# Kernel optimization log

Hardware: AMD Instinct MI355X
Metric: run time of the kernel (lower is better)

Reference implementation:

```python
import jax, jax.numpy as jnp
import numpy as np

N_NODES = 100000
N_EDGES = 1600000
IN_DIM = 128
HID = 64
N_CLASSES = 40
NEG_SLOPE = 0.2


def setup_inputs() -> dict:
    key = jax.random.key(0)
    ks = jax.random.split(key, 12)
    s_in = 1.0 / np.sqrt(IN_DIM)
    s_h = 1.0 / np.sqrt(HID)
    return {
        "x": jax.random.normal(ks[0], (N_NODES, IN_DIM), dtype=jnp.float32),
        "edge_index": jax.random.randint(ks[1], (2, N_EDGES), 0, N_NODES, dtype=jnp.int64),
        "W0": jax.random.normal(ks[2], (IN_DIM, HID), dtype=jnp.float32) * s_in,
        "a_s0": jax.random.normal(ks[3], (HID,), dtype=jnp.float32) * s_h,
        "a_d0": jax.random.normal(ks[4], (HID,), dtype=jnp.float32) * s_h,
        "b0": jnp.zeros((HID,), dtype=jnp.float32),
        "W1": jax.random.normal(ks[5], (HID, HID), dtype=jnp.float32) * s_h,
        "a_s1": jax.random.normal(ks[6], (HID,), dtype=jnp.float32) * s_h,
        "a_d1": jax.random.normal(ks[7], (HID,), dtype=jnp.float32) * s_h,
        "b1": jnp.zeros((HID,), dtype=jnp.float32),
        "Wl": jax.random.normal(ks[8], (HID, N_CLASSES), dtype=jnp.float32) * s_h,
        "bl": jnp.zeros((N_CLASSES,), dtype=jnp.float32),
    }


def gat_conv(x, src, dst, W, a_s, a_d, b, n_nodes):
    # single-head GATConv (PyG default heads=1), self-loops already in src/dst
    h = x @ W                                  # [N, d]
    e = jax.nn.leaky_relu((h @ a_s)[src] + (h @ a_d)[dst], NEG_SLOPE)  # [E]
    # segment softmax over incoming edges of each dst node
    m = jax.ops.segment_max(e, dst, num_segments=n_nodes)
    p = jnp.exp(e - m[dst])
    denom = jax.ops.segment_sum(p, dst, num_segments=n_nodes)
    alpha = p / (denom[dst] + 1e-16)           # [E]
    out = jax.ops.segment_sum(alpha[:, None] * h[src], dst, num_segments=n_nodes)
    return out + b


def reference(x, edge_index, W0, a_s0, a_d0, b0, W1, a_s1, a_d1, b1, Wl, bl):
    n = x.shape[0]
    loop = jnp.arange(n, dtype=edge_index.dtype)
    src = jnp.concatenate([edge_index[0], loop])
    dst = jnp.concatenate([edge_index[1], loop])
    h = gat_conv(x, src, dst, W0, a_s0, a_d0, b0, n)
    h = jax.nn.elu(h)
    h = gat_conv(h, src, dst, W1, a_s1, a_d1, b1, n)
    h = jax.nn.elu(h)
    return h @ Wl + bl
```

## Files before the change

### kernel.cpp

```cpp
#include <hip/hip_runtime.h>
#include <math.h>

#define NEG_SLOPE 0.2f
#define CAP 128
#define BSH 9
#define BSZ 512
#define CHUNK 4096
#define PADS 16
#define CAPQ 16384

typedef __attribute__((ext_vector_type(8))) short short8;
typedef __attribute__((ext_vector_type(4))) float f32x4;

__device__ __forceinline__ float hred_sum(float v) {
#pragma unroll
    for (int o = 16; o >= 1; o >>= 1) v += __shfl_xor(v, o, 64);
    return v;
}
__device__ __forceinline__ unsigned int f2bf(float f) {
    unsigned int u = __float_as_uint(f);
    return (u + 0x7fffu + ((u >> 16) & 1u)) >> 16;
}
__device__ __forceinline__ float bflo(unsigned int u) { return __uint_as_float(u << 16); }
__device__ __forceinline__ float bfhi(unsigned int u) { return __uint_as_float(u & 0xffff0000u); }

__device__ __forceinline__ void packw_body(const float* __restrict__ W, short* __restrict__ dst,
                                           int OUTW, int NKC, int NC) {
    int tot = NKC * NC * 64;
    for (int f = threadIdx.x; f < tot; f += 256) {
        int flane = f & 63;
        int fc    = (f >> 6) % NC;
        int fkc   = (f >> 6) / NC;
        int col   = fc * 16 + (flane & 15);
        int k0    = fkc * 32 + (flane >> 4) * 8;
        short8 b;
#pragma unroll
        for (int j = 0; j < 8; ++j) {
            float v = (col < OUTW) ? W[(k0 + j) * OUTW + col] : 0.f;
            b[j] = (short)f2bf(v);
        }
        *(short8*)&dst[f * 8] = b;
    }
}


__global__ __launch_bounds__(256) void k_scatter(
        const int* __restrict__ src, const int* __restrict__ dst,
        int* __restrict__ bcursor, int* __restrict__ ebuf, int E, int nscat,
        const float* __restrict__ W0, const float* __restrict__ W1,
        const float* __restrict__ Wl,
        short* __restrict__ wpk0, short* __restrict__ wpk1, short* __restrict__ wpkl) {
    __shared__ int lh[256], lb[256];
    const int tid = threadIdx.x;
    const int bid = blockIdx.x;
    if (bid >= nscat) {
        int role = bid - nscat;
        if (role == 0)      packw_body(W0, wpk0, 64, 4, 4);
        else if (role == 1) packw_body(W1, wpk1, 64, 2, 4);
        else                packw_body(Wl, wpkl, 40, 2, 3);
        return;
    }
    int base = bid * CHUNK;
    int sv[16], dv[16];
    bool ok[16];
#pragma unroll
    for (int u = 0; u < 16; ++u) {
        int i = base + u * 256 + tid;
        ok[u] = i < E;
        int ii = ok[u] ? i : E - 1;
        dv[u] = dst[ii];
        sv[u] = src[ii];
    }
    lh[tid] = 0;
    __syncthreads();
#pragma unroll
    for (int u = 0; u < 16; ++u)
        if (ok[u]) atomicAdd(&lh[dv[u] >> BSH], 1);
    __syncthreads();
    int c = lh[tid];
    lb[tid] = c ? atomicAdd(&bcursor[tid * PADS], c) : 0;
    lh[tid] = 0;
    __syncthreads();
#pragma unroll
    for (int u = 0; u < 16; ++u) {
        if (ok[u]) {
            int d = dv[u], b = d >> BSH;
            int pp = atomicAdd(&lh[b], 1);
            int pos = lb[b] + pp;
            if (pos < CAPQ)
                ebuf[b * CAPQ + pos] = (sv[u] << BSH) | (d & (BSZ - 1));
        }
    }
}


__device__ __forceinline__ void gemm0_body(char* smem, int bid,
        const float* __restrict__ X, const short* __restrict__ wpk,
        const float* __restrict__ a_s, const float* __restrict__ a_d,
        unsigned int* __restrict__ hb, float* __restrict__ ss, float* __restrict__ sd, int N) {
    constexpr int K = 128, OUTW = 64, NKC = K / 32, NC = OUTW / 16;
    short* wfrag = (short*)smem;
    unsigned int* hs = (unsigned int*)(smem + 16384);

    const int tid  = threadIdx.x;
    const int lane = tid & 63;
    const int w    = tid >> 6;
    const int m    = lane & 15;
    const int q8   = lane >> 4;
    const int rowbase = bid * 128 + w * 16;

    for (int f = tid; f < NKC * NC * 64; f += 512)
        *(uint4*)&wfrag[f * 8] = ((const uint4*)wpk)[f];
    __syncthreads();

    int grow = rowbase + m; if (grow >= N) grow = N - 1;

    f32x4 acc[NC];
#pragma unroll
    for (int c = 0; c < NC; ++c) acc[c] = (f32x4)0.f;

    const float* xrow = X + (size_t)grow * K + q8 * 8;
#pragma unroll
    for (int kc = 0; kc < NKC; ++kc) {
        float4 v0 = *(const float4*)(xrow + kc * 32);
        float4 v1 = *(const float4*)(xrow + kc * 32 + 4);
        float vv[8] = {v0.x, v0.y, v0.z, v0.w, v1.x, v1.y, v1.z, v1.w};
        short8 ah, al;
#pragma unroll
        for (int j = 0; j < 8; ++j) {
            unsigned int hb16 = f2bf(vv[j]);
            ah[j] = (short)hb16;
            al[j] = (short)f2bf(vv[j] - __uint_as_float(hb16 << 16));
        }
#pragma unroll
        for (int c = 0; c < NC; ++c) {
            short8 b = *(short8*)&wfrag[((kc * NC + c) * 64 + lane) * 8];
            acc[c] = __builtin_amdgcn_mfma_f32_16x16x32_bf16(ah, b, acc[c], 0, 0, 0);
            acc[c] = __builtin_amdgcn_mfma_f32_16x16x32_bf16(al, b, acc[c], 0, 0, 0);
        }
    }

    float asv[NC], adv[NC];
#pragma unroll
    for (int c = 0; c < NC; ++c) { asv[c] = a_s[c * 16 + m]; adv[c] = a_d[c * 16 + m]; }
#pragma unroll
    for (int i = 0; i < 4; ++i) {
        float s = 0.f, d = 0.f;
#pragma unroll
        for (int c = 0; c < NC; ++c) {
            s = fmaf(acc[c][i], asv[c], s);
            d = fmaf(acc[c][i], adv[c], d);
        }
#pragma unroll
        for (int o = 1; o <= 8; o <<= 1) {
            s += __shfl_xor(s, o, 64);
            d += __shfl_xor(d, o, 64);
        }
        int r = rowbase + q8 * 4 + i;
        if (m == 0 && r < N) { ss[r] = s; sd[r] = d; }
    }

    unsigned short* hsw = (unsigned short*)&hs[w * 512];
#pragma unroll
    for (int c = 0; c < NC; ++c)
#pragma unroll
        for (int i = 0; i < 4; ++i)
            hsw[(q8 * 4 + i) * 64 + c * 16 + m] = (unsigned short)f2bf(acc[c][i]);
    unsigned int* hu = &hs[w * 512];
    int row = lane >> 2, u0 = (lane & 3) * 8;
    uint4 va = *(uint4*)&hu[row * 32 + u0];
    uint4 vb = *(uint4*)&hu[row * 32 + u0 + 4];
    int r = rowbase + row;
    if (r < N) {
        *(uint4*)&hb[(size_t)r * 32 + u0]     = va;
        *(uint4*)&hb[(size_t)r * 32 + u0 + 4] = vb;
    }
}

__device__ __forceinline__ void build_body(char* smem, int b,
        const int* __restrict__ bcursor, const int* __restrict__ ebuf,
        int* __restrict__ rowptr, int* __restrict__ csr,
        int N, int nbuck) {
    int* sdeg  = (int*)smem;
    int* sscan = sdeg + 512;
    int* shdr  = sscan + 512;
    const int t = threadIdx.x;

    int nlo = b << BSH;
    int cn = N - nlo; if (cn > BSZ) cn = BSZ;

    int bcv = 0, totv = 0;
    if (t < 256) {
        int cnb = 0;
        if (t < nbuck) {
            bcv = bcursor[t * PADS]; if (bcv > CAPQ) bcv = CAPQ;
            cnb = N - (t << BSH); if (cnb > BSZ) cnb = BSZ; if (cnb < 0) cnb = 0;
        }
        totv = bcv + cnb;
        sscan[t] = totv;
    }
    __syncthreads();
#pragma unroll
    for (int off = 1; off < 256; off <<= 1) {
        int u = 0;
        if (t < 256 && t >= off) u = sscan[t - off];
        __syncthreads();
        if (t < 256) sscan[t] += u;
        __syncthreads();
    }
    if (t == b) { shdr[0] = sscan[t] - totv; shdr[1] = bcv; }
    if (b == 0 && t == nbuck - 1) rowptr[N] = sscan[t];
    __syncthreads();
    int cb = shdr[0], ec = shdr[1];
    int e0 = b * CAPQ;

    sdeg[t] = (t < cn) ? 1 : 0;
    __syncthreads();
    {
        int i = t;
        for (; i + 1536 < ec; i += 2048) {
            int r0 = ebuf[e0 + i], r1 = ebuf[e0 + i + 512];
            int r2 = ebuf[e0 + i + 1024], r3 = ebuf[e0 + i + 1536];
            atomicAdd(&sdeg[r0 & (BSZ - 1)], 1);
            atomicAdd(&sdeg[r1 & (BSZ - 1)], 1);
            atomicAdd(&sdeg[r2 & (BSZ - 1)], 1);
            atomicAdd(&sdeg[r3 & (BSZ - 1)], 1);
        }
        for (; i < ec; i += 512)
            atomicAdd(&sdeg[ebuf[e0 + i] & (BSZ - 1)], 1);
    }
    __syncthreads();
    int v = sdeg[t];
    sscan[t] = v;
    __syncthreads();
#pragma unroll
    for (int off = 1; off < BSZ; off <<= 1) {
        int u = (t >= off) ? sscan[t - off] : 0;
        __syncthreads();
        sscan[t] += u;
        __syncthreads();
    }
    int excl = sscan[t] - v;
    if (t < cn) {
        rowptr[nlo + t] = cb + excl;
        csr[cb + excl] = nlo + t;
        sdeg[t] = excl + 1;
    }
    __syncthreads();
    {
        int i = t;
        for (; i + 1536 < ec; i += 2048) {
            int r0 = ebuf[e0 + i], r1 = ebuf[e0 + i + 512];
            int r2 = ebuf[e0 + i + 1024], r3 = ebuf[e0 + i + 1536];
            int p0 = atomicAdd(&sdeg[r0 & (BSZ - 1)], 1);
            int p1 = atomicAdd(&sdeg[r1 & (BSZ - 1)], 1);
            int p2 = atomicAdd(&sdeg[r2 & (BSZ - 1)], 1);
            int p3 = atomicAdd(&sdeg[r3 & (BSZ - 1)], 1);
            csr[cb + p0] = r0 >> BSH;
            csr[cb + p1] = r1 >> BSH;
            csr[cb + p2] = r2 >> BSH;
            csr[cb + p3] = r3 >> BSH;
        }
        for (; i < ec; i += 512) {
            int rec = ebuf[e0 + i];
            int p = atomicAdd(&sdeg[rec & (BSZ - 1)], 1);
            csr[cb + p] = rec >> BSH;
        }
    }
}

__global__ __launch_bounds__(512) void k_mid(
        int* __restrict__ bcursor, int* __restrict__ ebuf, int gbm, int nbuck,
        const float* __restrict__ X, const short* __restrict__ wpk0,
        const float* __restrict__ a_s, const float* __restrict__ a_d,
        unsigned int* __restrict__ hb, float* __restrict__ ss, float* __restrict__ sd,
        int* __restrict__ rowptr, int* __restrict__ csr, int N) {
    __shared__ __align__(16) char smem[32768];
    int bid = blockIdx.x;
    if (bid < gbm)
        gemm0_body(smem, bid, X, wpk0, a_s, a_d, hb, ss, sd, N);
    else
        build_body(smem, bid - gbm, bcursor, ebuf, rowptr, csr, N, nbuck);
}


template <int OUTW, bool LAST>
__global__ __launch_bounds__(512) void k_aggmm(
        const int* __restrict__ rowptr, const int* __restrict__ csr,
        const float* __restrict__ ss, const float* __restrict__ sd,
        const unsigned int* __restrict__ hb, const float* __restrict__ bias,
        const short* __restrict__ wpk, const float* __restrict__ a_s2,
        const float* __restrict__ a_d2,
        unsigned int* __restrict__ hbout, float* __restrict__ ssout,
        float* __restrict__ sdout,
        const float* __restrict__ bias2, float* __restrict__ fout, int N) {
    constexpr int NKC = 2;
    constexpr int NC  = (OUTW + 15) / 16;
    __shared__ __align__(16) float sal[16][CAP];
    __shared__ __align__(16) int   sof[16][CAP];
    __shared__ __align__(16) short afrag[NKC][512];
    __shared__ __align__(16) unsigned short hsw[LAST ? 1 : 16][64];
    __shared__ float ssp[LAST ? 1 : NC][16], sdp[LAST ? 1 : NC][16];

    const int tid  = threadIdx.x;
    const int lane = tid & 63;
    const int w    = tid >> 6;
    const int m    = lane & 15;
    const int q8   = lane >> 4;

    short8 bq0, bq1;
    if (w < NC) {
        bq0 = *(const short8*)&wpk[((0 * NC + w) * 64 + lane) * 8];
        bq1 = *(const short8*)&wpk[((1 * NC + w) * 64 + lane) * 8];
    }

    const int hw = tid >> 5;
    const int p  = tid & 31;
    const int nb = blockIdx.x * 16;
    const int n  = nb + hw;
    const bool valid = n < N;
    const char* hbb = (const char*)hb;
    const int p4 = p * 4;

    int ro = 0, deg = 0;
    float sdn = 0.f;
    if (valid) {
        ro  = rowptr[n];
        deg = rowptr[n + 1] - ro;
        sdn = sd[n];
    }

    float fxr, fyr, inv;
    if (deg <= CAP) {
        float sum = 0.f;
        for (int j = p; j < deg; j += 32) {
            int s = csr[ro + j];
            float e = ss[s] + sdn;
            e = fmaxf(e, NEG_SLOPE * e);
            float pe = __expf(e);
            sal[hw][j] = pe;
            sof[hw][j] = s << 7;
            sum += pe;
        }
        sum = hred_sum(sum);
        inv = 1.f / (sum + 1e-16f);

        float ax = 0.f, ay = 0.f, bx = 0.f, by = 0.f, cx = 0.f, cy = 0.f, dx = 0.f, dy = 0.f;
        int j = 0;
        for (; j + 7 < deg; j += 8) {
            float4 al0 = *(const float4*)&sal[hw][j];
            float4 al1 = *(const float4*)&sal[hw][j + 4];
            int4   of0 = *(const int4*)&sof[hw][j];
            int4   of1 = *(const int4*)&sof[hw][j + 4];
            unsigned int u0 = *(const unsigned int*)(hbb + (of0.x + p4));
            unsigned int u1 = *(const unsigned int*)(hbb + (of0.y + p4));
            unsigned int u2 = *(const unsigned int*)(hbb + (of0.z + p4));
            unsigned int u3 = *(const unsigned int*)(hbb + (of0.w + p4));
            unsigned int u4 = *(const unsigned int*)(hbb + (of1.x + p4));
            unsigned int u5 = *(const unsigned int*)(hbb + (of1.y + p4));
            unsigned int u6 = *(const unsigned int*)(hbb + (of1.z + p4));
            unsigned int u7 = *(const unsigned int*)(hbb + (of1.w + p4));
            ax = fmaf(bflo(u0), al0.x, ax); ay = fmaf(bfhi(u0), al0.x, ay);
            bx = fmaf(bflo(u1), al0.y, bx); by = fmaf(bfhi(u1), al0.y, by);
            cx = fmaf(bflo(u2), al0.z, cx); cy = fmaf(bfhi(u2), al0.z, cy);
            dx = fmaf(bflo(u3), al0.w, dx); dy = fmaf(bfhi(u3), al0.w, dy);
            ax = fmaf(bflo(u4), al1.x, ax); ay = fmaf(bfhi(u4), al1.x, ay);
            bx = fmaf(bflo(u5), al1.y, bx); by = fmaf(bfhi(u5), al1.y, by);
            cx = fmaf(bflo(u6), al1.z, cx); cy = fmaf(bfhi(u6), al1.z, cy);
            dx = fmaf(bflo(u7), al1.w, dx); dy = fmaf(bfhi(u7), al1.w, dy);
        }
        for (; j + 3 < deg; j += 4) {
            float4 al0 = *(const float4*)&sal[hw][j];
            int4   of0 = *(const int4*)&sof[hw][j];
            unsigned int u0 = *(const unsigned int*)(hbb + (of0.x + p4));
            unsigned int u1 = *(const unsigned int*)(hbb + (of0.y + p4));
            unsigned int u2 = *(const unsigned int*)(hbb + (of0.z + p4));
            unsigned int u3 = *(const unsigned int*)(hbb + (of0.w + p4));
            ax = fmaf(bflo(u0), al0.x, ax); ay = fmaf(bfhi(u0), al0.x, ay);
            bx = fmaf(bflo(u1), al0.y, bx); by = fmaf(bfhi(u1), al0.y, by);
            cx = fmaf(bflo(u2), al0.z, cx); cy = fmaf(bfhi(u2), al0.z, cy);
            dx = fmaf(bflo(u3), al0.w, dx); dy = fmaf(bfhi(u3), al0.w, dy);
        }
        for (; j < deg; ++j) {
            float a = sal[hw][j];
            unsigned int u0 = *(const unsigned int*)(hbb + (sof[hw][j] + p4));
            ax = fmaf(bflo(u0), a, ax); ay = fmaf(bfhi(u0), a, ay);
        }
        fxr = (ax + bx) + (cx + dx);
        fyr = (ay + by) + (cy + dy);
    } else {
        float sum = 0.f;
        for (int j = p; j < deg; j += 32) {
            int s = csr[ro + j];
            float e = ss[s] + sdn;
            e = fmaxf(e, NEG_SLOPE * e);
            sum += __expf(e);
        }
        sum = hred_sum(sum);
        inv = 1.f / (sum + 1e-16f);
        float fx = 0.f, fy = 0.f;
        for (int j = 0; j < deg; ++j) {
            int s = csr[ro + j];
            float e = ss[s] + sdn;
            e = fmaxf(e, NEG_SLOPE * e);
            float pe = __expf(e);
            unsigned int u = *(const unsigned int*)(hbb + ((s << 7) + p4));
            fx = fmaf(bflo(u), pe, fx); fy = fmaf(bfhi(u), pe, fy);
        }
        fxr = fx; fyr = fy;
    }
    {
        float2 ob = *(const float2*)&bias[p * 2];
        float ox = fmaf(fxr, inv, ob.x);
        float oy = fmaf(fyr, inv, ob.y);
        ox = (ox > 0.f) ? ox : __expf(ox) - 1.f;
        oy = (oy > 0.f) ? oy : __expf(oy) - 1.f;
        unsigned int zu = (f2bf(oy) << 16) | f2bf(ox);
        int k   = 2 * p;
        int kc  = k >> 5;
        int idx = ((((k & 31) >> 3) * 16 + hw) << 3) + (k & 7);
        *(unsigned int*)&afrag[kc][idx] = zu;
    }
    __syncthreads();

    if (w < NC) {
        f32x4 acc = (f32x4)0.f;
        {
            short8 a0 = *(short8*)&afrag[0][lane * 8];
            acc = __builtin_amdgcn_mfma_f32_16x16x32_bf16(a0, bq0, acc, 0, 0, 0);
            short8 a1 = *(short8*)&afrag[1][lane * 8];
            acc = __builtin_amdgcn_mfma_f32_16x16x32_bf16(a1, bq1, acc, 0, 0, 0);
        }
        if constexpr (LAST) {
#pragma unroll
            for (int i = 0; i < 4; ++i) {
                int r = nb + q8 * 4 + i;
                int col = w * 16 + m;
                if (r < N && col < OUTW)
                    fout[(size_t)r * OUTW + col] = acc[i] + bias2[col];
            }
        } else {
            float asv = a_s2[w * 16 + m];
            float adv = a_d2[w * 16 + m];
#pragma unroll
            for (int i = 0; i < 4; ++i) {
                float s = acc[i] * asv, d = acc[i] * adv;
#pragma unroll
                for (int o = 1; o <= 8; o <<= 1) {
                    s += __shfl_xor(s, o, 64);
                    d += __shfl_xor(d, o, 64);
                }
                if (m == 0) { ssp[w][q8 * 4 + i] = s; sdp[w][q8 * 4 + i] = d; }
                hsw[q8 * 4 + i][w * 16 + m] = (unsigned short)f2bf(acc[i]);
            }
        }
    }
    if constexpr (!LAST) {
        __syncthreads();
        if (tid < 16) {
            int r = nb + tid;
            if (r < N) {
                float s = 0.f, d = 0.f;
#pragma unroll
                for (int c = 0; c < NC; ++c) { s += ssp[c][tid]; d += sdp[c][tid]; }
                ssout[r] = s; sdout[r] = d;
            }
        }
        if (tid < 128) {
            int row = tid >> 3, seg = tid & 7;
            int r = nb + row;
            if (r < N) {
                uint4 v = *(uint4*)&((unsigned int*)hsw)[row * 32 + seg * 4];
                *(uint4*)&hbout[(size_t)r * 32 + seg * 4] = v;
            }
        }
    }
}


extern "C" void kernel_launch(void* const* d_in, const int* in_sizes, int n_in,
                              void* d_out, int out_size, void* d_ws, size_t ws_size,
                              hipStream_t stream) {
    const float* x   = (const float*)d_in[0];
    const int*   ei  = (const int*)d_in[1];
    const float* W0  = (const float*)d_in[2];
    const float* as0 = (const float*)d_in[3];
    const float* ad0 = (const float*)d_in[4];
    const float* b0  = (const float*)d_in[5];
    const float* W1  = (const float*)d_in[6];
    const float* as1 = (const float*)d_in[7];
    const float* ad1 = (const float*)d_in[8];
    const float* b1  = (const float*)d_in[9];
    const float* Wl  = (const float*)d_in[10];
    const float* bl  = (const float*)d_in[11];
    float* out = (float*)d_out;

    int N = in_sizes[0] / 128;
    int E = in_sizes[1] / 2;
    const int* srcp = ei;
    const int* dstp = ei + E;
    int nbuck = (N + BSZ - 1) >> BSH;

    char* wp = (char*)d_ws;
    auto alloc = [&](size_t bytes) { void* p = (void*)wp; wp += (bytes + 255) & ~(size_t)255; return p; };
    unsigned int* hb0 = (unsigned int*)alloc((size_t)N * 32 * 4);
    unsigned int* hb1 = (unsigned int*)alloc((size_t)N * 32 * 4);
    float* ss0     = (float*)alloc((size_t)N * 4);
    float* sd0     = (float*)alloc((size_t)N * 4);
    float* ss1     = (float*)alloc((size_t)N * 4);
    float* sd1     = (float*)alloc((size_t)N * 4);
    int*   rowptr  = (int*)alloc((size_t)(N + 1) * 4);
    int*   csr     = (int*)alloc((size_t)(E + N) * 4);
    int*   ebuf    = (int*)alloc((size_t)nbuck * CAPQ * 4);
    int*   bcursor = (int*)alloc(256 * PADS * 4);
    short* wpk0    = (short*)alloc(4 * 4 * 64 * 8 * 2);
    short* wpk1    = (short*)alloc(2 * 4 * 64 * 8 * 2);
    short* wpkl    = (short*)alloc(2 * 3 * 64 * 8 * 2);

    int nscat = (E + CHUNK - 1) / CHUNK;
    int gbm   = (N + 127) / 128;
    int gagg  = (N + 15) / 16;

    hipMemsetAsync(bcursor, 0, 256 * PADS * 4, stream);
    k_scatter<<<nscat + 3, 256, 0, stream>>>(srcp, dstp, bcursor, ebuf, E, nscat,
                                             W0, W1, Wl, wpk0, wpk1, wpkl);
    k_mid<<<gbm + nbuck, 512, 0, stream>>>(bcursor, ebuf, gbm, nbuck,
                                           x, wpk0, as0, ad0, hb0, ss0, sd0,
                                           rowptr, csr, N);

    k_aggmm<64, false><<<gagg, 512, 0, stream>>>(rowptr, csr, ss0, sd0, hb0, b0,
                                                 wpk1, as1, ad1,
                                                 hb1, ss1, sd1, nullptr, nullptr, N);
    k_aggmm<40, true><<<gagg, 512, 0, stream>>>(rowptr, csr, ss1, sd1, hb1, b1,
                                                wpkl, nullptr, nullptr,
                                                nullptr, nullptr, nullptr, bl, out, N);
}
```

Measured before the change: 238.0 us.

## Remap aggregation so each lane accumulates 16 features directly into MFMA A-fragments

Restructures the aggregate-then-matmul kernel. Previously a half-wave of 32 lanes handled one node, with 2 features per lane. Now a wavefront handles 16 nodes, with 4 lanes per node each holding 16 features in registers. The accumulated features feed the MFMA A operand directly, with no shared-memory staging or block barrier. This removes the LDS alpha/offset buffers, the cross-lane softmax reduction and the __syncthreads. In exchange, lanes within a wave now walk different degree lists, so they diverge, and each lane issues a dependent uint4 gather per edge. Block size drops to 256 with 64 nodes per block.

```diff
diff --git a/kernel.cpp b/kernel.cpp
--- a/kernel.cpp
+++ b/kernel.cpp
@@ -2,7 +2,6 @@
 #include <math.h>
 
 #define NEG_SLOPE 0.2f
-#define CAP 128
 #define BSH 9
 #define BSZ 512
 #define CHUNK 4096
@@ -12,11 +11,6 @@
 typedef __attribute__((ext_vector_type(8))) short short8;
 typedef __attribute__((ext_vector_type(4))) float f32x4;
 
-__device__ __forceinline__ float hred_sum(float v) {
-#pragma unroll
-    for (int o = 16; o >= 1; o >>= 1) v += __shfl_xor(v, o, 64);
-    return v;
-}
 __device__ __forceinline__ unsigned int f2bf(float f) {
     unsigned int u = __float_as_uint(f);
     return (u + 0x7fffu + ((u >> 16) & 1u)) >> 16;
@@ -285,7 +279,7 @@
 
 
 template <int OUTW, bool LAST>
-__global__ __launch_bounds__(512) void k_aggmm(
+__global__ __launch_bounds__(256) void k_aggmm(
         const int* __restrict__ rowptr, const int* __restrict__ csr,
         const float* __restrict__ ss, const float* __restrict__ sd,
         const unsigned int* __restrict__ hb, const float* __restrict__ bias,
@@ -294,33 +288,17 @@
         unsigned int* __restrict__ hbout, float* __restrict__ ssout,
         float* __restrict__ sdout,
         const float* __restrict__ bias2, float* __restrict__ fout, int N) {
-    constexpr int NKC = 2;
-    constexpr int NC  = (OUTW + 15) / 16;
-    __shared__ __align__(16) float sal[16][CAP];
-    __shared__ __align__(16) int   sof[16][CAP];
-    __shared__ __align__(16) short afrag[NKC][512];
-    __shared__ __align__(16) unsigned short hsw[LAST ? 1 : 16][64];
-    __shared__ float ssp[LAST ? 1 : NC][16], sdp[LAST ? 1 : NC][16];
+    constexpr int NC = (OUTW + 15) / 16;
+    __shared__ __align__(16) unsigned int hs[LAST ? 1 : 4][512];
 
     const int tid  = threadIdx.x;
     const int lane = tid & 63;
     const int w    = tid >> 6;
     const int m    = lane & 15;
-    const int q8   = lane >> 4;
-
-    short8 bq0, bq1;
-    if (w < NC) {
-        bq0 = *(const short8*)&wpk[((0 * NC + w) * 64 + lane) * 8];
-        bq1 = *(const short8*)&wpk[((1 * NC + w) * 64 + lane) * 8];
-    }
-
-    const int hw = tid >> 5;
-    const int p  = tid & 31;
-    const int nb = blockIdx.x * 16;
-    const int n  = nb + hw;
+    const int q    = lane >> 4;
+    const int nb16 = (blockIdx.x * 4 + w) * 16;
+    const int n    = nb16 + m;
     const bool valid = n < N;
-    const char* hbb = (const char*)hb;
-    const int p4 = p * 4;
 
     int ro = 0, deg = 0;
     float sdn = 0.f;
@@ -330,149 +308,121 @@
         sdn = sd[n];
     }
 
-    float fxr, fyr, inv;
-    if (deg <= CAP) {
-        float sum = 0.f;
-        for (int j = p; j < deg; j += 32) {
-            int s = csr[ro + j];
-            float e = ss[s] + sdn;
-            e = fmaxf(e, NEG_SLOPE * e);
-            float pe = __expf(e);
-            sal[hw][j] = pe;
-            sof[hw][j] = s << 7;
-            sum += pe;
-        }
-        sum = hred_sum(sum);
-        inv = 1.f / (sum + 1e-16f);
-
-        float ax = 0.f, ay = 0.f, bx = 0.f, by = 0.f, cx = 0.f, cy = 0.f, dx = 0.f, dy = 0.f;
-        int j = 0;
-        for (; j + 7 < deg; j += 8) {
-            float4 al0 = *(const float4*)&sal[hw][j];
-            float4 al1 = *(const float4*)&sal[hw][j + 4];
-            int4   of0 = *(const int4*)&sof[hw][j];
-            int4   of1 = *(const int4*)&sof[hw][j + 4];
-            unsigned int u0 = *(const unsigned int*)(hbb + (of0.x + p4));
-            unsigned int u1 = *(const unsigned int*)(hbb + (of0.y + p4));
-            unsigned int u2 = *(const unsigned int*)(hbb + (of0.z + p4));
-            unsigned int u3 = *(const unsigned int*)(hbb + (of0.w + p4));
-            unsigned int u4 = *(const unsigned int*)(hbb + (of1.x + p4));
-            unsigned int u5 = *(const unsigned int*)(hbb + (of1.y + p4));
-            unsigned int u6 = *(const unsigned int*)(hbb + (of1.z + p4));
-            unsigned int u7 = *(const unsigned int*)(hbb + (of1.w + p4));
-            ax = fmaf(bflo(u0), al0.x, ax); ay = fmaf(bfhi(u0), al0.x, ay);
-            bx = fmaf(bflo(u1), al0.y, bx); by = fmaf(bfhi(u1), al0.y, by);
-            cx = fmaf(bflo(u2), al0.z, cx); cy = fmaf(bfhi(u2), al0.z, cy);
-            dx = fmaf(bflo(u3), al0.w, dx); dy = fmaf(bfhi(u3), al0.w, dy);
-            ax = fmaf(bflo(u4), al1.x, ax); ay = fmaf(bfhi(u4), al1.x, ay);
-            bx = fmaf(bflo(u5), al1.y, bx); by = fmaf(bfhi(u5), al1.y, by);
-            cx = fmaf(bflo(u6), al1.z, cx); cy = fmaf(bfhi(u6), al1.z, cy);
-            dx = fmaf(bflo(u7), al1.w, dx); dy = fmaf(bfhi(u7), al1.w, dy);
-        }
-        for (; j + 3 < deg; j += 4) {
-            float4 al0 = *(const float4*)&sal[hw][j];
-            int4   of0 = *(const int4*)&sof[hw][j];
-            unsigned int u0 = *(const unsigned int*)(hbb + (of0.x + p4));
-            unsigned int u1 = *(const unsigned int*)(hbb + (of0.y + p4));
-            unsigned int u2 = *(const unsigned int*)(hbb + (of0.z + p4));
-            unsigned int u3 = *(const unsigned int*)(hbb + (of0.w + p4));
-            ax = fmaf(bflo(u0), al0.x, ax); ay = fmaf(bfhi(u0), al0.x, ay);
-            bx = fmaf(bflo(u1), al0.y, bx); by = fmaf(bfhi(u1), al0.y, by);
-            cx = fmaf(bflo(u2), al0.z, cx); cy = fmaf(bfhi(u2), al0.z, cy);
-            dx = fmaf(bflo(u3), al0.w, dx); dy = fmaf(bfhi(u3), al0.w, dy);
-        }
-        for (; j < deg; ++j) {
-            float a = sal[hw][j];
-            unsigned int u0 = *(const unsigned int*)(hbb + (sof[hw][j] + p4));
-            ax = fmaf(bflo(u0), a, ax); ay = fmaf(bfhi(u0), a, ay);
-        }
-        fxr = (ax + bx) + (cx + dx);
-        fyr = (ay + by) + (cy + dy);
+    float f0=0.f,f1=0.f,f2=0.f,f3=0.f,f4=0.f,f5=0.f,f6=0.f,f7=0.f;
+    float f8=0.f,f9=0.f,f10=0.f,f11=0.f,f12=0.f,f13=0.f,f14=0.f,f15=0.f;
+    float sum = 0.f;
+
+#define ACC16(UA, UB, PE) \
+    f0  = fmaf(bflo(UA.x), PE, f0);  f1  = fmaf(bfhi(UA.x), PE, f1);  \
+    f2  = fmaf(bflo(UA.y), PE, f2);  f3  = fmaf(bfhi(UA.y), PE, f3);  \
+    f4  = fmaf(bflo(UA.z), PE, f4);  f5  = fmaf(bfhi(UA.z), PE, f5);  \
+    f6  = fmaf(bflo(UA.w), PE, f6);  f7  = fmaf(bfhi(UA.w), PE, f7);  \
+    f8  = fmaf(bflo(UB.x), PE, f8);  f9  = fmaf(bfhi(UB.x), PE, f9);  \
+    f10 = fmaf(bflo(UB.y), PE, f10); f11 = fmaf(bfhi(UB.y), PE, f11); \
+    f12 = fmaf(bflo(UB.z), PE, f12); f13 = fmaf(bfhi(UB.z), PE, f13); \
+    f14 = fmaf(bflo(UB.w), PE, f14); f15 = fmaf(bfhi(UB.w), PE, f15)
+
+    int j = 0;
+    for (; j + 1 < deg; j += 2) {
+        int s0 = csr[ro + j], s1 = csr[ro + j + 1];
+        float e0 = ss[s0] + sdn, e1 = ss[s1] + sdn;
+        e0 = fmaxf(e0, NEG_SLOPE * e0); e1 = fmaxf(e1, NEG_SLOPE * e1);
+        float p0 = __expf(e0), p1 = __expf(e1);
+        sum += p0; sum += p1;
+        const uint4* r0 = (const uint4*)(hb + (size_t)s0 * 32);
+        const uint4* r1 = (const uint4*)(hb + (size_t)s1 * 32);
+        uint4 ua0 = r0[q], ub0 = r0[4 + q];
+        uint4 ua1 = r1[q], ub1 = r1[4 + q];
+        ACC16(ua0, ub0, p0);
+        ACC16(ua1, ub1, p1);
+    }
+    for (; j < deg; ++j) {
+        int s0 = csr[ro + j];
+        float e0 = ss[s0] + sdn;
+        e0 = fmaxf(e0, NEG_SLOPE * e0);
+        float p0 = __expf(e0);
+        sum += p0;
+        const uint4* r0 = (const uint4*)(hb + (size_t)s0 * 32);
+        uint4 ua0 = r0[q], ub0 = r0[4 + q];
+        ACC16(ua0, ub0, p0);
+    }
+#undef ACC16
+
+    float inv = 1.f / (sum + 1e-16f);
+
+    float4 bA0 = *(const float4*)&bias[q * 8];
+    float4 bA1 = *(const float4*)&bias[q * 8 + 4];
+    float4 bB0 = *(const float4*)&bias[32 + q * 8];
+    float4 bB1 = *(const float4*)&bias[32 + q * 8 + 4];
+    short8 a0, a1;
+    {
+        float o;
+#define ZP(DST, IDX, F, B) \
+        o = fmaf(F, inv, B); o = (o > 0.f) ? o : __expf(o) - 1.f; DST[IDX] = (short)f2bf(o)
+        ZP(a0, 0, f0,  bA0.x); ZP(a0, 1, f1,  bA0.y); ZP(a0, 2, f2,  bA0.z); ZP(a0, 3, f3,  bA0.w);
+        ZP(a0, 4, f4,  bA1.x); ZP(a0, 5, f5,  bA1.y); ZP(a0, 6, f6,  bA1.z); ZP(a0, 7, f7,  bA1.w);
+        ZP(a1, 0, f8,  bB0.x); ZP(a1, 1, f9,  bB0.y); ZP(a1, 2, f10, bB0.z); ZP(a1, 3, f11, bB0.w);
+        ZP(a1, 4, f12, bB1.x); ZP(a1, 5, f13, bB1.y); ZP(a1, 6, f14, bB1.z); ZP(a1, 7, f15, bB1.w);
+#undef ZP
+    }
+
+    f32x4 acc[NC];
+#pragma unroll
+    for (int c = 0; c < NC; ++c) acc[c] = (f32x4)0.f;
+#pragma unroll
+    for (int c = 0; c < NC; ++c) {
+        short8 b0 = *(const short8*)&wpk[((0 * NC + c) * 64 + lane) * 8];
+        acc[c] = __builtin_amdgcn_mfma_f32_16x16x32_bf16(a0, b0, acc[c], 0, 0, 0);
+        short8 b1 = *(const short8*)&wpk[((1 * NC + c) * 64 + lane) * 8];
+        acc[c] = __builtin_amdgcn_mfma_f32_16x16x32_bf16(a1, b1, acc[c], 0, 0, 0);
+    }
+
+    if constexpr (LAST) {
+#pragma unroll
+        for (int i = 0; i < 4; ++i) {
+            int r = nb16 + q * 4 + i;
+            if (r < N) {
+#pragma unroll
+                for (int c = 0; c < NC; ++c) {
+                    int col = c * 16 + m;
+                    if (col < OUTW) fout[(size_t)r * OUTW + col] = acc[c][i] + bias2[col];
+                }
+            }
+        }
     } else {
-        float sum = 0.f;
-        for (int j = p; j < deg; j += 32) {
-            int s = csr[ro + j];
-            float e = ss[s] + sdn;
-            e = fmaxf(e, NEG_SLOPE * e);
-            sum += __expf(e);
-        }
-        sum = hred_sum(sum);
-        inv = 1.f / (sum + 1e-16f);
-        float fx = 0.f, fy = 0.f;
-        for (int j = 0; j < deg; ++j) {
-            int s = csr[ro + j];
-            float e = ss[s] + sdn;
-            e = fmaxf(e, NEG_SLOPE * e);
-            float pe = __expf(e);
-            unsigned int u = *(const unsigned int*)(hbb + ((s << 7) + p4));
-            fx = fmaf(bflo(u), pe, fx); fy = fmaf(bfhi(u), pe, fy);
-        }
-        fxr = fx; fyr = fy;
-    }
-    {
-        float2 ob = *(const float2*)&bias[p * 2];
-        float ox = fmaf(fxr, inv, ob.x);
-        float oy = fmaf(fyr, inv, ob.y);
-        ox = (ox > 0.f) ? ox : __expf(ox) - 1.f;
-        oy = (oy > 0.f) ? oy : __expf(oy) - 1.f;
-        unsigned int zu = (f2bf(oy) << 16) | f2bf(ox);
-        int k   = 2 * p;
-        int kc  = k >> 5;
-        int idx = ((((k & 31) >> 3) * 16 + hw) << 3) + (k & 7);
-        *(unsigned int*)&afrag[kc][idx] = zu;
-    }
-    __syncthreads();
-
-    if (w < NC) {
-        f32x4 acc = (f32x4)0.f;
-        {
-            short8 a0 = *(short8*)&afrag[0][lane * 8];
-            acc = __builtin_amdgcn_mfma_f32_16x16x32_bf16(a0, bq0, acc, 0, 0, 0);
-            short8 a1 = *(short8*)&afrag[1][lane * 8];
-            acc = __builtin_amdgcn_mfma_f32_16x16x32_bf16(a1, bq1, acc, 0, 0, 0);
-        }
-        if constexpr (LAST) {
-#pragma unroll
-            for (int i = 0; i < 4; ++i) {
-                int r = nb + q8 * 4 + i;
-                int col = w * 16 + m;
-                if (r < N && col < OUTW)
-                    fout[(size_t)r * OUTW + col] = acc[i] + bias2[col];
+        float asv[NC], adv[NC];
+#pragma unroll
+        for (int c = 0; c < NC; ++c) { asv[c] = a_s2[c * 16 + m]; adv[c] = a_d2[c * 16 + m]; }
+#pragma unroll
+        for (int i = 0; i < 4; ++i) {
+            float s = 0.f, d = 0.f;
+#pragma unroll
+            for (int c = 0; c < NC; ++c) {
+                s = fmaf(acc[c][i], asv[c], s);
+                d = fmaf(acc[c][i], adv[c], d);
             }
-        } else {
-            float asv = a_s2[w * 16 + m];
-            float adv = a_d2[w * 16 + m];
-#pragma unroll
-            for (int i = 0; i < 4; ++i) {
-                float s = acc[i] * asv, d = acc[i] * adv;
-#pragma unroll
-                for (int o = 1; o <= 8; o <<= 1) {
-                    s += __shfl_xor(s, o, 64);
-                    d += __shfl_xor(d, o, 64);
-                }
-                if (m == 0) { ssp[w][q8 * 4 + i] = s; sdp[w][q8 * 4 + i] = d; }
-                hsw[q8 * 4 + i][w * 16 + m] = (unsigned short)f2bf(acc[i]);
+#pragma unroll
+            for (int o = 1; o <= 8; o <<= 1) {
+                s += __shfl_xor(s, o, 64);
+                d += __shfl_xor(d, o, 64);
             }
-        }
-    }
-    if constexpr (!LAST) {
-        __syncthreads();
-        if (tid < 16) {
-            int r = nb + tid;
-            if (r < N) {
-                float s = 0.f, d = 0.f;
-#pragma unroll
-                for (int c = 0; c < NC; ++c) { s += ssp[c][tid]; d += sdp[c][tid]; }
-                ssout[r] = s; sdout[r] = d;
-            }
-        }
-        if (tid < 128) {
-            int row = tid >> 3, seg = tid & 7;
-            int r = nb + row;
-            if (r < N) {
-                uint4 v = *(uint4*)&((unsigned int*)hsw)[row * 32 + seg * 4];
-                *(uint4*)&hbout[(size_t)r * 32 + seg * 4] = v;
-            }
+            int r = nb16 + q * 4 + i;
+            if (m == 0 && r < N) { ssout[r] = s; sdout[r] = d; }
+        }
+        unsigned short* hsw = (unsigned short*)&hs[w][0];
+#pragma unroll
+        for (int c = 0; c < NC; ++c)
+#pragma unroll
+            for (int i = 0; i < 4; ++i)
+                hsw[(q * 4 + i) * 64 + c * 16 + m] = (unsigned short)f2bf(acc[c][i]);
+        unsigned int* hu = &hs[w][0];
+        int row = lane >> 2, u0 = (lane & 3) * 8;
+        uint4 va = *(uint4*)&hu[row * 32 + u0];
+        uint4 vb = *(uint4*)&hu[row * 32 + u0 + 4];
+        int r = nb16 + row;
+        if (r < N) {
+            *(uint4*)&hbout[(size_t)r * 32 + u0]     = va;
+            *(uint4*)&hbout[(size_t)r * 32 + u0 + 4] = vb;
         }
     }
 }
@@ -519,7 +469,7 @@
 
     int nscat = (E + CHUNK - 1) / CHUNK;
     int gbm   = (N + 127) / 128;
-    int gagg  = (N + 15) / 16;
+    int gagg  = (N + 63) / 64;
 
     hipMemsetAsync(bcursor, 0, 256 * PADS * 4, stream);
     k_scatter<<<nscat + 3, 256, 0, stream>>>(srcp, dstp, bcursor, ebuf, E, nscat,
@@ -528,10 +478,10 @@
                                            x, wpk0, as0, ad0, hb0, ss0, sd0,
                                            rowptr, csr, N);
 
-    k_aggmm<64, false><<<gagg, 512, 0, stream>>>(rowptr, csr, ss0, sd0, hb0, b0,
+    k_aggmm<64, false><<<gagg, 256, 0, stream>>>(rowptr, csr, ss0, sd0, hb0, b0,
                                                  wpk1, as1, ad1,
                                                  hb1, ss1, sd1, nullptr, nullptr, N);
-    k_aggmm<40, true><<<gagg, 512, 0, stream>>>(rowptr, csr, ss1, sd1, hb1, b1,
+    k_aggmm<40, true><<<gagg, 256, 0, stream>>>(rowptr, csr, ss1, sd1, hb1, b1,
                                                 wpkl, nullptr, nullptr,
                                                 nullptr, nullptr, nullptr, bl, out, N);
 }
```

Result: slower. 242.8 us (+2.0%).
